# Kernel optimization log

Measured on AMD Instinct MI355X. Metric: run time of the kernel, lower is better.

Reference implementation:

```python
import jax, jax.numpy as jnp
import numpy as np

B, C, N, RATIO = 16, 1024, 16384, 8
BN_EPS = 1e-5


def setup_inputs() -> dict:
    key = jax.random.key(0)
    k1, k2, k3, k4 = jax.random.split(key, 4)
    return {
        "x": jax.random.normal(k1, (B, C, N), dtype=jnp.float32),
        "w1": jax.random.normal(k2, (C // RATIO, C), dtype=jnp.float32) * (1.0 / np.sqrt(C)),
        "w2": jax.random.normal(k3, (C, C // RATIO), dtype=jnp.float32) * (1.0 / np.sqrt(C // RATIO)),
        "sw": jax.random.normal(k4, (2,), dtype=jnp.float32),
        "gamma": jnp.ones((1,), dtype=jnp.float32),
        "beta": jnp.zeros((1,), dtype=jnp.float32),
        "running_mean": jnp.zeros((1,), dtype=jnp.float32),
        "running_var": jnp.ones((1,), dtype=jnp.float32),
    }


def reference(x, w1, w2, sw, gamma, beta, running_mean, running_var):
    # ---- Channel attention (CBAM) ----
    m = jnp.mean(x, axis=-1)   # (B, C) avg pool over N
    mx = jnp.max(x, axis=-1)   # (B, C) max pool over N

    def mlp(v):  # shared Conv1d(k=1) MLP: C -> C/r -> C
        h = jax.nn.relu(jnp.einsum('rc,bc->br', w1, v))
        return jnp.einsum('cr,br->bc', w2, h)

    gate = jax.nn.sigmoid(mlp(m) + mlp(mx))[:, :, None]  # (B, C, 1)
    x1 = gate * x                                          # (B, C, N)

    # ---- Spatial attention ----
    cm = jnp.mean(x1, axis=1, keepdims=True)  # (B, 1, N) mean over C
    cx = jnp.max(x1, axis=1, keepdims=True)   # (B, 1, N) max over C
    # torch concat order is [max, mean]; conv1 weight sw applies accordingly
    s = sw[0] * cx + sw[1] * cm               # (B, 1, N)
    # BatchNorm1d(1) in eval mode with running stats
    s = (s - running_mean[0]) * jax.lax.rsqrt(running_var[0] + BN_EPS) * gamma[0] + beta[0]
    s = jax.nn.relu(s)
    att = jax.nn.softmax(s, axis=-1)          # softmax over N
    return att * x1                            # (B, C, N)
```

## Files before the change

### kernel.cpp

```cpp
#include <hip/hip_runtime.h>
#include <math.h>

#define BB 16
#define CC 1024
#define NN 16384
#define HID 128
#define SPLIT 4
#define CPART (CC/SPLIT)
#define N4 (NN/4)
#define EXPSHIFT 10.0f

__global__ __launch_bounds__(256) void k1_pool(const float* __restrict__ x,
                                               float* __restrict__ meanp,
                                               float* __restrict__ maxp) {
    const int row = blockIdx.x;
    const int tid = threadIdx.x;
    const float4* xr = (const float4*)(x + (size_t)row * NN);
    float s = 0.f, m = -INFINITY;
    #pragma unroll
    for (int i = 0; i < 16; ++i) {
        float4 v = xr[tid + i * 256];
        s += v.x + v.y + v.z + v.w;
        m = fmaxf(m, fmaxf(fmaxf(v.x, v.y), fmaxf(v.z, v.w)));
    }
    __shared__ float ss[4], sm[4];
    for (int off = 32; off > 0; off >>= 1) {
        s += __shfl_down(s, off, 64);
        m = fmaxf(m, __shfl_down(m, off, 64));
    }
    const int wave = tid >> 6, lane = tid & 63;
    if (lane == 0) { ss[wave] = s; sm[wave] = m; }
    __syncthreads();
    if (tid == 0) {
        float fs = ss[0] + ss[1] + ss[2] + ss[3];
        float fm = fmaxf(fmaxf(sm[0], sm[1]), fmaxf(sm[2], sm[3]));
        meanp[row] = fs * (1.0f / NN);
        maxp[row]  = fm;
    }
}

__global__ __launch_bounds__(1024) void k2_gate(const float* __restrict__ meanp,
                                                const float* __restrict__ maxp,
                                                const float* __restrict__ w1,
                                                const float* __restrict__ w2,
                                                float* __restrict__ gate) {
    const int b = blockIdx.x;
    const int tid = threadIdx.x;
    __shared__ float sv[2][CC];
    __shared__ float hh[2][HID];
    __shared__ float h[HID];
    if (tid < CC) {
        sv[0][tid] = meanp[b * CC + tid];
        sv[1][tid] = maxp[b * CC + tid];
    }
    __syncthreads();
    {
        const int slot = tid >> 2;
        const int part = tid & 3;
        const int src  = slot >> 7;
        const int r    = slot & 127;
        const float* w1r = w1 + (size_t)r * CC;
        const float* svp = sv[src];
        float acc = 0.f;
        const int c0 = part * 256;
        #pragma unroll 8
        for (int c = c0; c < c0 + 256; ++c) acc = fmaf(w1r[c], svp[c], acc);
        acc += __shfl_xor(acc, 1, 64);
        acc += __shfl_xor(acc, 2, 64);
        if (part == 0) hh[src][r] = fmaxf(acc, 0.f);
    }
    __syncthreads();
    if (tid < HID) h[tid] = hh[0][tid] + hh[1][tid];
    __syncthreads();
    {
        const float* w2r = w2 + (size_t)tid * HID;
        float a = 0.f;
        #pragma unroll
        for (int r = 0; r < HID; ++r) a = fmaf(w2r[r], h[r], a);
        gate[b * CC + tid] = 1.0f / (1.0f + expf(-a));
    }
}

__global__ __launch_bounds__(256) void k3_spatial(const float* __restrict__ x,
                                                  const float* __restrict__ gate,
                                                  float* __restrict__ psum,
                                                  float* __restrict__ pmax) {
    const int chunk = blockIdx.x;
    const int split = blockIdx.y;
    const int b     = blockIdx.z;
    const int tid = threadIdx.x;
    __shared__ float g[CPART];
    g[tid] = gate[b * CC + split * CPART + tid];
    __syncthreads();
    const int n4 = chunk * 256 + tid;
    const float4* xb = (const float4*)(x + ((size_t)b * CC + (size_t)split * CPART) * NN);
    float4 s = {0.f, 0.f, 0.f, 0.f};
    float4 m = {-INFINITY, -INFINITY, -INFINITY, -INFINITY};
    #pragma unroll 8
    for (int c = 0; c < CPART; ++c) {
        float4 v = xb[(size_t)c * N4 + n4];
        float gc = g[c];
        s.x = fmaf(gc, v.x, s.x);
        s.y = fmaf(gc, v.y, s.y);
        s.z = fmaf(gc, v.z, s.z);
        s.w = fmaf(gc, v.w, s.w);
        m.x = fmaxf(m.x, gc * v.x);
        m.y = fmaxf(m.y, gc * v.y);
        m.z = fmaxf(m.z, gc * v.z);
        m.w = fmaxf(m.w, gc * v.w);
    }
    const size_t o = (size_t)(b * SPLIT + split) * N4 + n4;
    ((float4*)psum)[o] = s;
    ((float4*)pmax)[o] = m;
}

__global__ __launch_bounds__(256) void k4_exp(const float* __restrict__ psum,
                                              const float* __restrict__ pmax,
                                              const float* __restrict__ sw,
                                              const float* __restrict__ gamma,
                                              const float* __restrict__ beta,
                                              const float* __restrict__ rmean,
                                              const float* __restrict__ rvar,
                                              float* __restrict__ attexp,
                                              float* __restrict__ blksum) {
    const int chunk = blockIdx.x;
    const int b     = blockIdx.y;
    const int tid = threadIdx.x;
    const float sw0 = sw[0], sw1 = sw[1];
    const float scale = gamma[0] * rsqrtf(rvar[0] + 1e-5f);
    const float shift = beta[0] - rmean[0] * scale;
    const int i = chunk * 256 + tid;
    const float4* ps = (const float4*)psum;
    const float4* pm = (const float4*)pmax;
    float4 ssum = {0.f, 0.f, 0.f, 0.f};
    float4 smax = {-INFINITY, -INFINITY, -INFINITY, -INFINITY};
    #pragma unroll
    for (int sp = 0; sp < SPLIT; ++sp) {
        float4 a = ps[(size_t)(b * SPLIT + sp) * N4 + i];
        float4 c = pm[(size_t)(b * SPLIT + sp) * N4 + i];
        ssum.x += a.x; ssum.y += a.y; ssum.z += a.z; ssum.w += a.w;
        smax.x = fmaxf(smax.x, c.x); smax.y = fmaxf(smax.y, c.y);
        smax.z = fmaxf(smax.z, c.z); smax.w = fmaxf(smax.w, c.w);
    }
    auto sval = [&](float su, float mx) -> float {
        float v = sw0 * mx + sw1 * (su * (1.0f / CC));
        v = fmaf(v, scale, shift);
        v = fmaxf(v, 0.f);
        return expf(v - EXPSHIFT);
    };
    float4 e;
    e.x = sval(ssum.x, smax.x);
    e.y = sval(ssum.y, smax.y);
    e.z = sval(ssum.z, smax.z);
    e.w = sval(ssum.w, smax.w);
    ((float4*)attexp)[(size_t)b * N4 + i] = e;
    float lsum = e.x + e.y + e.z + e.w;
    for (int off = 32; off > 0; off >>= 1) lsum += __shfl_down(lsum, off, 64);
    __shared__ float red[4];
    if ((tid & 63) == 0) red[tid >> 6] = lsum;
    __syncthreads();
    if (tid == 0) blksum[b * 16 + chunk] = red[0] + red[1] + red[2] + red[3];
}

__global__ __launch_bounds__(256) void k6_final(const float* __restrict__ x,
                                                const float* __restrict__ gate,
                                                const float* __restrict__ attexp,
                                                const float* __restrict__ blksum,
                                                float* __restrict__ out) {
    const int blk = blockIdx.x;
    const int t = blk & 3;
    const int row = blk >> 2;
    const int b = row >> 10;
    const int tid = threadIdx.x;
    float tot = 0.f;
    #pragma unroll
    for (int j = 0; j < 16; ++j) tot += blksum[b * 16 + j];
    const float gsc = gate[row] / tot;
    const size_t base4  = (size_t)row * N4 + t * 1024 + tid;
    const size_t abase4 = (size_t)b * N4 + t * 1024 + tid;
    const float4* xp = (const float4*)x;
    const float4* ap = (const float4*)attexp;
    float4* op = (float4*)out;
    #pragma unroll
    for (int j = 0; j < 4; ++j) {
        float4 v = xp[base4 + j * 256];
        float4 a = ap[abase4 + j * 256];
        float4 o;
        o.x = v.x * a.x * gsc;
        o.y = v.y * a.y * gsc;
        o.z = v.z * a.z * gsc;
        o.w = v.w * a.w * gsc;
        op[base4 + j * 256] = o;
    }
}

extern "C" void kernel_launch(void* const* d_in, const int* in_sizes, int n_in,
                              void* d_out, int out_size, void* d_ws, size_t ws_size,
                              hipStream_t stream) {
    const float* x     = (const float*)d_in[0];
    const float* w1    = (const float*)d_in[1];
    const float* w2    = (const float*)d_in[2];
    const float* sw    = (const float*)d_in[3];
    const float* gamma = (const float*)d_in[4];
    const float* beta  = (const float*)d_in[5];
    const float* rmean = (const float*)d_in[6];
    const float* rvar  = (const float*)d_in[7];
    float* out = (float*)d_out;
    float* ws  = (float*)d_ws;

    float* meanp  = ws;
    float* maxp   = meanp + 16384;
    float* gate   = maxp + 16384;
    float* psum   = gate + 16384;
    float* pmax   = psum + (size_t)BB * SPLIT * NN;
    float* attexp = pmax + (size_t)BB * SPLIT * NN;
    float* blksum = attexp + (size_t)BB * NN;

    k1_pool<<<BB * CC, 256, 0, stream>>>(x, meanp, maxp);
    k2_gate<<<BB, 1024, 0, stream>>>(meanp, maxp, w1, w2, gate);
    dim3 g3(NN / 1024, SPLIT, BB);
    k3_spatial<<<g3, 256, 0, stream>>>(x, gate, psum, pmax);
    dim3 g4(16, BB);
    k4_exp<<<g4, 256, 0, stream>>>(psum, pmax, sw, gamma, beta, rmean, rvar, attexp, blksum);
    k6_final<<<BB * CC * 4, 256, 0, stream>>>(x, gate, attexp, blksum, out);
}
```

Baseline: 811.0 us.

## Use nontemporal loads/stores, precompute gate scale, and regroup final kernel by channel groups

Adds nontemporal load and store builtins on the large streaming reads of x in the pool, spatial and final kernels, and on the output writes. Adds a small kernel that precomputes gate/softmax-sum per row, so the final kernel no longer sums the per-block totals in every block. The final kernel is re-gridded so each thread reuses one attention vector across 8 channel rows and issues 8 independent loads. It also raises the unroll in the spatial reduction. This adds one kernel launch, and the nontemporal hints may interfere with L2/MALL reuse of x between passes.

```diff
diff --git a/kernel.cpp b/kernel.cpp
--- a/kernel.cpp
+++ b/kernel.cpp
@@ -9,17 +9,20 @@
 #define CPART (CC/SPLIT)
 #define N4 (NN/4)
 #define EXPSHIFT 10.0f
+#define CG 8
+
+typedef float f4 __attribute__((ext_vector_type(4)));
 
 __global__ __launch_bounds__(256) void k1_pool(const float* __restrict__ x,
                                                float* __restrict__ meanp,
                                                float* __restrict__ maxp) {
     const int row = blockIdx.x;
     const int tid = threadIdx.x;
-    const float4* xr = (const float4*)(x + (size_t)row * NN);
+    const f4* xr = (const f4*)(x + (size_t)row * NN);
     float s = 0.f, m = -INFINITY;
     #pragma unroll
     for (int i = 0; i < 16; ++i) {
-        float4 v = xr[tid + i * 256];
+        f4 v = __builtin_nontemporal_load(&xr[tid + i * 256]);
         s += v.x + v.y + v.z + v.w;
         m = fmaxf(m, fmaxf(fmaxf(v.x, v.y), fmaxf(v.z, v.w)));
     }
@@ -93,12 +96,12 @@
     g[tid] = gate[b * CC + split * CPART + tid];
     __syncthreads();
     const int n4 = chunk * 256 + tid;
-    const float4* xb = (const float4*)(x + ((size_t)b * CC + (size_t)split * CPART) * NN);
-    float4 s = {0.f, 0.f, 0.f, 0.f};
-    float4 m = {-INFINITY, -INFINITY, -INFINITY, -INFINITY};
-    #pragma unroll 8
+    const f4* xb = (const f4*)(x + ((size_t)b * CC + (size_t)split * CPART) * NN);
+    f4 s = {0.f, 0.f, 0.f, 0.f};
+    f4 m = {-INFINITY, -INFINITY, -INFINITY, -INFINITY};
+    #pragma unroll 16
     for (int c = 0; c < CPART; ++c) {
-        float4 v = xb[(size_t)c * N4 + n4];
+        f4 v = __builtin_nontemporal_load(&xb[(size_t)c * N4 + n4]);
         float gc = g[c];
         s.x = fmaf(gc, v.x, s.x);
         s.y = fmaf(gc, v.y, s.y);
@@ -110,8 +113,8 @@
         m.w = fmaxf(m.w, gc * v.w);
     }
     const size_t o = (size_t)(b * SPLIT + split) * N4 + n4;
-    ((float4*)psum)[o] = s;
-    ((float4*)pmax)[o] = m;
+    ((f4*)psum)[o] = s;
+    ((f4*)pmax)[o] = m;
 }
 
 __global__ __launch_bounds__(256) void k4_exp(const float* __restrict__ psum,
@@ -130,14 +133,14 @@
     const float scale = gamma[0] * rsqrtf(rvar[0] + 1e-5f);
     const float shift = beta[0] - rmean[0] * scale;
     const int i = chunk * 256 + tid;
-    const float4* ps = (const float4*)psum;
-    const float4* pm = (const float4*)pmax;
-    float4 ssum = {0.f, 0.f, 0.f, 0.f};
-    float4 smax = {-INFINITY, -INFINITY, -INFINITY, -INFINITY};
+    const f4* ps = (const f4*)psum;
+    const f4* pm = (const f4*)pmax;
+    f4 ssum = {0.f, 0.f, 0.f, 0.f};
+    f4 smax = {-INFINITY, -INFINITY, -INFINITY, -INFINITY};
     #pragma unroll
     for (int sp = 0; sp < SPLIT; ++sp) {
-        float4 a = ps[(size_t)(b * SPLIT + sp) * N4 + i];
-        float4 c = pm[(size_t)(b * SPLIT + sp) * N4 + i];
+        f4 a = ps[(size_t)(b * SPLIT + sp) * N4 + i];
+        f4 c = pm[(size_t)(b * SPLIT + sp) * N4 + i];
         ssum.x += a.x; ssum.y += a.y; ssum.z += a.z; ssum.w += a.w;
         smax.x = fmaxf(smax.x, c.x); smax.y = fmaxf(smax.y, c.y);
         smax.z = fmaxf(smax.z, c.z); smax.w = fmaxf(smax.w, c.w);
@@ -148,12 +151,12 @@
         v = fmaxf(v, 0.f);
         return expf(v - EXPSHIFT);
     };
-    float4 e;
+    f4 e;
     e.x = sval(ssum.x, smax.x);
     e.y = sval(ssum.y, smax.y);
     e.z = sval(ssum.z, smax.z);
     e.w = sval(ssum.w, smax.w);
-    ((float4*)attexp)[(size_t)b * N4 + i] = e;
+    ((f4*)attexp)[(size_t)b * N4 + i] = e;
     float lsum = e.x + e.y + e.z + e.w;
     for (int off = 32; off > 0; off >>= 1) lsum += __shfl_down(lsum, off, 64);
     __shared__ float red[4];
@@ -162,35 +165,45 @@
     if (tid == 0) blksum[b * 16 + chunk] = red[0] + red[1] + red[2] + red[3];
 }
 
+__global__ __launch_bounds__(256) void k5_gscale(const float* __restrict__ gate,
+                                                 const float* __restrict__ blksum,
+                                                 float* __restrict__ gscale) {
+    const int row = blockIdx.x * 256 + threadIdx.x;
+    const int b = row >> 10;
+    float tot = 0.f;
+    #pragma unroll
+    for (int j = 0; j < 16; ++j) tot += blksum[b * 16 + j];
+    gscale[row] = gate[row] / tot;
+}
+
 __global__ __launch_bounds__(256) void k6_final(const float* __restrict__ x,
-                                                const float* __restrict__ gate,
+                                                const float* __restrict__ gscale,
                                                 const float* __restrict__ attexp,
-                                                const float* __restrict__ blksum,
                                                 float* __restrict__ out) {
-    const int blk = blockIdx.x;
-    const int t = blk & 3;
-    const int row = blk >> 2;
-    const int b = row >> 10;
-    const int tid = threadIdx.x;
-    float tot = 0.f;
-    #pragma unroll
-    for (int j = 0; j < 16; ++j) tot += blksum[b * 16 + j];
-    const float gsc = gate[row] / tot;
-    const size_t base4  = (size_t)row * N4 + t * 1024 + tid;
-    const size_t abase4 = (size_t)b * N4 + t * 1024 + tid;
-    const float4* xp = (const float4*)x;
-    const float4* ap = (const float4*)attexp;
-    float4* op = (float4*)out;
-    #pragma unroll
-    for (int j = 0; j < 4; ++j) {
-        float4 v = xp[base4 + j * 256];
-        float4 a = ap[abase4 + j * 256];
-        float4 o;
-        o.x = v.x * a.x * gsc;
-        o.y = v.y * a.y * gsc;
-        o.z = v.z * a.z * gsc;
-        o.w = v.w * a.w * gsc;
-        op[base4 + j * 256] = o;
+    const int chunk = blockIdx.x;
+    const int cgrp  = blockIdx.y;
+    const int b     = blockIdx.z;
+    const int tid = threadIdx.x;
+    const int n4 = chunk * 256 + tid;
+    const int row0 = b * CC + cgrp * CG;
+    const f4 a = ((const f4*)attexp)[(size_t)b * N4 + n4];
+    float gs[CG];
+    #pragma unroll
+    for (int r = 0; r < CG; ++r) gs[r] = gscale[row0 + r];
+    const f4* xp = (const f4*)x;
+    f4* op = (f4*)out;
+    f4 v[CG];
+    #pragma unroll
+    for (int r = 0; r < CG; ++r)
+        v[r] = __builtin_nontemporal_load(&xp[(size_t)(row0 + r) * N4 + n4]);
+    #pragma unroll
+    for (int r = 0; r < CG; ++r) {
+        f4 o;
+        o.x = v[r].x * a.x * gs[r];
+        o.y = v[r].y * a.y * gs[r];
+        o.z = v[r].z * a.z * gs[r];
+        o.w = v[r].w * a.w * gs[r];
+        __builtin_nontemporal_store(o, &op[(size_t)(row0 + r) * N4 + n4]);
     }
 }
 
@@ -211,7 +224,8 @@
     float* meanp  = ws;
     float* maxp   = meanp + 16384;
     float* gate   = maxp + 16384;
-    float* psum   = gate + 16384;
+    float* gscale = gate + 16384;
+    float* psum   = gscale + 16384;
     float* pmax   = psum + (size_t)BB * SPLIT * NN;
     float* attexp = pmax + (size_t)BB * SPLIT * NN;
     float* blksum = attexp + (size_t)BB * NN;
@@ -222,5 +236,7 @@
     k3_spatial<<<g3, 256, 0, stream>>>(x, gate, psum, pmax);
     dim3 g4(16, BB);
     k4_exp<<<g4, 256, 0, stream>>>(psum, pmax, sw, gamma, beta, rmean, rvar, attexp, blksum);
-    k6_final<<<BB * CC * 4, 256, 0, stream>>>(x, gate, attexp, blksum, out);
-}
+    k5_gscale<<<BB * CC / 256, 256, 0, stream>>>(gate, blksum, gscale);
+    dim3 g6(16, CC / CG, BB);
+    k6_final<<<g6, 256, 0, stream>>>(x, gscale, attexp, out);
+}
```

Result: faster. 758.8 us (-6.4%).
